# Kernel optimization log

Hardware: AMD Instinct MI355X
Metric: run time of the kernel (lower is better)

## Reference

```python
import jax, jax.numpy as jnp
import numpy as np
from math import pi as PI

K = 32
CUTOFF = 10.0
F = 128          # num_filters (also num_gaussians)
H = 256          # in_channels
N_CLASSES = 7
N_IND = 8
LOG2 = float(np.log(2.0))


def _ssp(x):
    # ShiftedSoftplus
    return jax.nn.softplus(x) - LOG2


def _gaussian_smearing(d):
    # d: [E, 1] -> [E, F]; torch_geometric GaussianSmearing(start=0, stop=cutoff)
    offset = jnp.linspace(0.0, CUTOFF, F, dtype=d.dtype)            # [F]
    coeff = -0.5 / (offset[1] - offset[0]) ** 2
    return jnp.exp(coeff * (d - offset[None, :]) ** 2)


def setup_inputs() -> dict:
    key = jax.random.key(0)
    ks = jax.random.split(key, 24)
    Nq, Nc, B = 8192, 16384, 8
    box = 20.0
    pos_query = jax.random.uniform(ks[0], (Nq, 3), dtype=jnp.float32) * box
    pos_ctx = jax.random.uniform(ks[1], (Nc, 3), dtype=jnp.float32) * box
    node_attr_ctx = jax.random.normal(ks[2], (Nc, H), dtype=jnp.float32)
    batch_query = jnp.sort(jax.random.randint(ks[3], (Nq,), 0, B)).astype(jnp.int32)
    batch_ctx = jnp.sort(jax.random.randint(ks[4], (Nc,), 0, B)).astype(jnp.int32)

    def lin_w(k, fin, fout):
        return (jax.random.normal(k, (fin, fout), dtype=jnp.float32) / np.sqrt(fin)).astype(jnp.float32)

    return {
        "pos_query": pos_query,
        "pos_ctx": pos_ctx,
        "node_attr_ctx": node_attr_ctx,
        "batch_query": batch_query,
        "batch_ctx": batch_ctx,
        "lin1_w": lin_w(ks[5], H, F),                 # bias=False
        "lin2_w": lin_w(ks[6], F, F),
        "lin2_b": jnp.zeros((F,), jnp.float32),
        "nn1_w": lin_w(ks[7], F, F),
        "nn1_b": jnp.zeros((F,), jnp.float32),
        "nn2_w": lin_w(ks[8], F, F),
        "nn2_b": jnp.zeros((F,), jnp.float32),
        "cls1_w": lin_w(ks[9], F, F),
        "cls1_b": jnp.zeros((F,), jnp.float32),
        "cls2_w": lin_w(ks[10], F, N_CLASSES),
        "cls2_b": jnp.zeros((N_CLASSES,), jnp.float32),
        "prop1_w": lin_w(ks[11], F, F),
        "prop1_b": jnp.zeros((F,), jnp.float32),
        "prop2_w": lin_w(ks[12], F, N_IND),
        "prop2_b": jnp.zeros((N_IND,), jnp.float32),
    }


def reference(pos_query, pos_ctx, node_attr_ctx, batch_query, batch_ctx,
              lin1_w, lin2_w, lin2_b, nn1_w, nn1_b, nn2_w, nn2_b,
              cls1_w, cls1_b, cls2_w, cls2_b, prop1_w, prop1_b, prop2_w, prop2_b):
    Nq = pos_query.shape[0]

    # --- batch-aware kNN: for each query, k nearest context points in same graph ---
    d2 = (jnp.sum(pos_query ** 2, -1)[:, None]
          + jnp.sum(pos_ctx ** 2, -1)[None, :]
          - 2.0 * (pos_query @ pos_ctx.T))                            # [Nq, Nc]
    same = batch_query[:, None] == batch_ctx[None, :]
    d2 = jnp.where(same, d2, jnp.inf)
    _, nbr = jax.lax.top_k(-d2, K)                                    # [Nq, K] ctx indices

    # --- gather neighbor data; each query owns exactly K contiguous edges ---
    diff = pos_query[:, None, :] - pos_ctx[nbr]                       # [Nq, K, 3]
    dist = jnp.sqrt(jnp.sum(diff ** 2, -1)).reshape(-1, 1)            # [E, 1]
    attr_j = node_attr_ctx[nbr].reshape(Nq * K, -1)                   # [E, H]

    # --- per-edge filter network on distance expansion ---
    W = _ssp(_gaussian_smearing(dist) @ nn1_w + nn1_b) @ nn2_w + nn2_b  # [E, F]

    h = (W * (attr_j @ lin1_w)) @ lin2_w + lin2_b                     # [E, F]

    # --- cosine cutoff envelope ---
    C = 0.5 * (jnp.cos(dist * (PI / CUTOFF)) + 1.0)
    C = C * (dist <= CUTOFF) * (dist >= 0.0)
    h = h * C                                                         # [E, F]

    # scatter_add by query index == sum over the K contiguous edges per query
    y = jnp.sum(h.reshape(Nq, K, F), axis=1)                          # [Nq, F]

    y_cls = _ssp(y @ cls1_w + cls1_b) @ cls2_w + cls2_b               # [Nq, 7]
    y_ind = _ssp(y @ prop1_w + prop1_b) @ prop2_w + prop2_b           # [Nq, 8]
    return (y_cls, y_ind)
```

## Files before the change

kernel.cpp:

```cpp
#include <hip/hip_runtime.h>
#include <math.h>

#define K 32
#define F 128
#define H 256
#define TAB 4096
#define QB 8
#define BMAX 16
#define RCUT2 100.0f
#define KBINS 64
#define BINCAP 2560
#define BCAP 128
#define FP 132
#define FRR 32
#define WRR 16

__device__ __forceinline__ float ssp(float x) {
    return fmaxf(x, 0.0f) + log1pf(expf(-fabsf(x))) - 0.69314718055994531f;
}

__device__ __forceinline__ float d2f4(float4 p, float qx, float qy, float qz) {
    float dx = qx - p.x;
    float dy = qy - p.y;
    float dz = qz - p.z;
    return fmaf(dz, dz, fmaf(dy, dy, dx * dx));
}

__global__ __launch_bounds__(256) void prep_kernel(const int* __restrict__ bc, int Nc,
                                                   int* __restrict__ ctx_start,
                                                   const float* __restrict__ posc,
                                                   float4* __restrict__ posc4) {
    int blk = blockIdx.x;
    int tid = threadIdx.x;
    if (blk == 0) {
        if (tid <= BMAX) {
            int b = tid;
            int lo = 0, hi = Nc;
            while (lo < hi) {
                int mid = (lo + hi) >> 1;
                if (bc[mid] < b) lo = mid + 1; else hi = mid;
            }
            ctx_start[b] = lo;
        }
    } else {
        int i = (blk - 1) * 256 + tid;
        if (i < Nc)
            posc4[i] = make_float4(posc[i * 3 + 0], posc[i * 3 + 1], posc[i * 3 + 2], 0.0f);
    }
}

__global__ __launch_bounds__(256) void feat_kernel(const float* __restrict__ attr,
                                                   const float* __restrict__ lin1_w,
                                                   float* __restrict__ ctx_feat, int Nc) {
    __shared__ float sa[FRR][H];
    int blk = blockIdx.x;
    int tid = threadIdx.x;
    int r0 = blk * FRR;
    int f = tid & 63;
    int g = tid >> 6;

    {
        float4* dst = (float4*)sa;
        const int total = FRR * H / 4;
        if (r0 + FRR <= Nc) {
            const float4* src = (const float4*)(attr + (size_t)r0 * H);
            for (int i = tid; i < total; i += 256) dst[i] = src[i];
        } else {
            for (int i = tid; i < total; i += 256) {
                int r = i / (H / 4);
                if (r0 + r < Nc) dst[i] = ((const float4*)(attr + (size_t)r0 * H))[i];
                else dst[i] = make_float4(0.0f, 0.0f, 0.0f, 0.0f);
            }
        }
    }
    __syncthreads();

    float acc0[8], acc1[8];
#pragma unroll
    for (int r = 0; r < 8; ++r) { acc0[r] = 0.0f; acc1[r] = 0.0f; }
    for (int k = 0; k < H; k += 4) {
        float wa0 = lin1_w[(k + 0) * F + f];
        float wa1 = lin1_w[(k + 1) * F + f];
        float wa2 = lin1_w[(k + 2) * F + f];
        float wa3 = lin1_w[(k + 3) * F + f];
        float wb0 = lin1_w[(k + 0) * F + f + 64];
        float wb1 = lin1_w[(k + 1) * F + f + 64];
        float wb2 = lin1_w[(k + 2) * F + f + 64];
        float wb3 = lin1_w[(k + 3) * F + f + 64];
#pragma unroll
        for (int r = 0; r < 8; ++r) {
            float4 a4 = *(const float4*)&sa[g * 8 + r][k];
            acc0[r] = fmaf(a4.x, wa0, acc0[r]);
            acc0[r] = fmaf(a4.y, wa1, acc0[r]);
            acc0[r] = fmaf(a4.z, wa2, acc0[r]);
            acc0[r] = fmaf(a4.w, wa3, acc0[r]);
            acc1[r] = fmaf(a4.x, wb0, acc1[r]);
            acc1[r] = fmaf(a4.y, wb1, acc1[r]);
            acc1[r] = fmaf(a4.z, wb2, acc1[r]);
            acc1[r] = fmaf(a4.w, wb3, acc1[r]);
        }
    }
#pragma unroll
    for (int r = 0; r < 8; ++r) {
        int row = r0 + g * 8 + r;
        if (row < Nc) {
            ctx_feat[(size_t)row * F + f] = acc0[r];
            ctx_feat[(size_t)row * F + f + 64] = acc1[r];
        }
    }
}

__global__ __launch_bounds__(256) void knn_kernel(const float* __restrict__ posq,
                                                  const float4* __restrict__ posc4,
                                                  const int* __restrict__ bq,
                                                  const int* __restrict__ ctx_start,
                                                  int* __restrict__ nbr, int Nq) {
    __shared__ unsigned char sbin[4][BINCAP];
    __shared__ int hist[4][KBINS];
    __shared__ unsigned bkey[4][BCAP];
    __shared__ int bidx[4][BCAP];
    __shared__ int s_nwin[4], s_nbnd[4];

    int tid = threadIdx.x;
    int lane = tid & 63;
    int w = tid >> 6;
    int q = blockIdx.x * 4 + w;
    bool active = q < Nq;
    int qc = active ? q : 0;

    hist[w][lane] = 0;
    if (lane == 0) { s_nwin[w] = 0; s_nbnd[w] = 0; }

    float qx = posq[qc * 3 + 0];
    float qy = posq[qc * 3 + 1];
    float qz = posq[qc * 3 + 2];
    int b = bq[qc];
    int c0 = ctx_start[b];
    int c1 = ctx_start[b + 1];
    int seg = active ? (c1 - c0) : 0;
    __syncthreads();

    const float SCALE = (float)KBINS / RCUT2;
    int farc = -1;

    for (int i = lane; i < seg; i += 64) {
        float d2 = d2f4(posc4[c0 + i], qx, qy, qz);
        int bin = 255;
        if (d2 < RCUT2) {
            bin = (int)(d2 * SCALE);
            atomicAdd(&hist[w][bin], 1);
        }
        if (i < BINCAP) sbin[w][i] = (unsigned char)bin;
    }
    __syncthreads();

    int h = hist[w][lane];
    int inc = h;
#pragma unroll
    for (int off = 1; off < 64; off <<= 1) {
        int v = __shfl_up(inc, off);
        if (lane >= off) inc += v;
    }
    unsigned long long bal = __ballot(inc >= K);
    int T, below;
    if (bal) {
        T = __ffsll(bal) - 1;
        below = __shfl(inc, T) - __shfl(h, T);
    } else {
        T = KBINS;
        below = __shfl(inc, 63);
    }

    for (int i = lane; i < seg; i += 64) {
        int c = c0 + i;
        int bin;
        if (i < BINCAP) bin = sbin[w][i];
        else {
            float d2 = d2f4(posc4[c], qx, qy, qz);
            bin = (d2 < RCUT2) ? (int)(d2 * SCALE) : 255;
        }
        if (bin < T) {
            int p = atomicAdd(&s_nwin[w], 1);
            nbr[(size_t)q * K + p] = c;
        } else if (bin == T) {
            int p = atomicAdd(&s_nbnd[w], 1);
            if (p < BCAP) {
                float d2 = d2f4(posc4[c], qx, qy, qz);
                bkey[w][p] = __float_as_uint(d2);
                bidx[w][p] = c;
            }
        } else if (bin == 255) {
            farc = c;
        }
    }
#pragma unroll
    for (int off = 1; off < 64; off <<= 1) farc = max(farc, __shfl_xor(farc, off));
    if (farc < 0) farc = c0;
    __syncthreads();

    if (!active) return;
    int nb = min(s_nbnd[w], BCAP);
    int m = K - s_nwin[w];
    for (int it = 0; it < m; ++it) {
        unsigned long long bestkey = 0xFFFFFFFFFFFFFFFFull;
        int bestp = -1;
        for (int p = lane; p < nb; p += 64) {
            unsigned kk = bkey[w][p];
            if (kk != 0xFFFFFFFFu) {
                unsigned long long pk = ((unsigned long long)kk << 32) | (unsigned)bidx[w][p];
                if (pk < bestkey) { bestkey = pk; bestp = p; }
            }
        }
#pragma unroll
        for (int off = 1; off < 64; off <<= 1) {
            unsigned long long ok = __shfl_xor(bestkey, off);
            int op = __shfl_xor(bestp, off);
            if (ok < bestkey) { bestkey = ok; bestp = op; }
        }
        if (lane == 0) {
            if (bestp >= 0 && bestkey != 0xFFFFFFFFFFFFFFFFull) {
                nbr[(size_t)q * K + below + it] = (int)(bestkey & 0xFFFFFFFFu);
                bkey[w][bestp] = 0xFFFFFFFFu;
            } else {
                nbr[(size_t)q * K + below + it] = farc;
            }
        }
        __asm__ volatile("" ::: "memory");
    }
}

__global__ __launch_bounds__(256) void wtab_kernel(const float* __restrict__ nn1_w,
                                                   const float* __restrict__ nn1_b,
                                                   const float* __restrict__ nn2_w,
                                                   const float* __restrict__ nn2_b,
                                                   float2* __restrict__ wt2) {
    __shared__ float sg[17][F];
    __shared__ float st[17][F];
    int t0 = blockIdx.x * WRR;
    int tid = threadIdx.x;
    int f = tid & (F - 1);
    int g = tid >> 7;

    const float delta = 10.0f / 127.0f;
    const float coeff = -0.5f / (delta * delta);
    float off = (float)f * delta;
    for (int r = g; r < 17; r += 2) {
        float dist = (float)(t0 + r) * (10.0f / (float)TAB);
        float d = dist - off;
        sg[r][f] = expf(coeff * d * d);
    }
    __syncthreads();

    float acc[9];
#pragma unroll
    for (int r = 0; r < 9; ++r) acc[r] = 0.0f;
    for (int j = 0; j < F; j += 4) {
        float w0 = nn1_w[(j + 0) * F + f];
        float w1 = nn1_w[(j + 1) * F + f];
        float w2 = nn1_w[(j + 2) * F + f];
        float w3 = nn1_w[(j + 3) * F + f];
#pragma unroll
        for (int r = 0; r < 9; ++r) {
            float4 a4 = *(const float4*)&sg[g * 8 + r][j];
            acc[r] = fmaf(a4.x, w0, acc[r]);
            acc[r] = fmaf(a4.y, w1, acc[r]);
            acc[r] = fmaf(a4.z, w2, acc[r]);
            acc[r] = fmaf(a4.w, w3, acc[r]);
        }
    }
    float b1 = nn1_b[f];
#pragma unroll
    for (int r = 0; r < 9; ++r) st[g * 8 + r][f] = ssp(acc[r] + b1);
    __syncthreads();

#pragma unroll
    for (int r = 0; r < 9; ++r) acc[r] = 0.0f;
    for (int j = 0; j < F; j += 4) {
        float w0 = nn2_w[(j + 0) * F + f];
        float w1 = nn2_w[(j + 1) * F + f];
        float w2 = nn2_w[(j + 2) * F + f];
        float w3 = nn2_w[(j + 3) * F + f];
#pragma unroll
        for (int r = 0; r < 9; ++r) {
            float4 a4 = *(const float4*)&st[g * 8 + r][j];
            acc[r] = fmaf(a4.x, w0, acc[r]);
            acc[r] = fmaf(a4.y, w1, acc[r]);
            acc[r] = fmaf(a4.z, w2, acc[r]);
            acc[r] = fmaf(a4.w, w3, acc[r]);
        }
    }
    float b2 = nn2_b[f];
#pragma unroll
    for (int i = 0; i < 8; ++i) {
        int t = t0 + g * 8 + i;
        wt2[(size_t)t * F + f] = make_float2(acc[i] + b2, acc[i + 1] + b2);
    }
}

__global__ __launch_bounds__(256) void agghead_kernel(const float* __restrict__ posq,
                                                      const float4* __restrict__ posc4,
                                                      const int* __restrict__ nbr,
                                                      const float* __restrict__ ctx_feat,
                                                      const float2* __restrict__ wt2,
                                                      const float* __restrict__ lin2_w,
                                                      const float* __restrict__ lin2_b,
                                                      const float* __restrict__ cls1_w,
                                                      const float* __restrict__ cls1_b,
                                                      const float* __restrict__ cls2_w,
                                                      const float* __restrict__ cls2_b,
                                                      const float* __restrict__ prop1_w,
                                                      const float* __restrict__ prop1_b,
                                                      const float* __restrict__ prop2_w,
                                                      const float* __restrict__ prop2_b,
                                                      float* __restrict__ out_cls,
                                                      float* __restrict__ out_ind, int Nq) {
    const int QH = QB / 2;
    int q0 = blockIdx.x * QB;
    int tid = threadIdx.x;

    __shared__ __align__(16) char sm[12672];
    float4* sedge      = (float4*)sm;
    float (*sa)[F]     = (float (*)[F])(sm + 4096);
    float* ssc         = (float*)(sm + 8192);
    float (*sc1)[FP]   = (float (*)[FP])(sm);
    float (*sp1)[FP]   = (float (*)[FP])(sm + 4224);
    float (*sy)[FP]    = (float (*)[FP])(sm + 8448);

    {
        int qq = tid >> 5;
        int q = q0 + qq;
        if (q >= Nq) q = Nq - 1;
        int j = nbr[(size_t)q * K + (tid & 31)];
        float4 p = posc4[j];
        float dx = posq[q * 3 + 0] - p.x;
        float dy = posq[q * 3 + 1] - p.y;
        float dz = posq[q * 3 + 2] - p.z;
        float dist = sqrtf(fmaf(dz, dz, fmaf(dy, dy, dx * dx)));
        float C = 0.0f, fr = 0.0f;
        int i0 = 0;
        if (dist <= 10.0f) {
            C = 0.5f * (cosf(dist * 0.31415926535897931f) + 1.0f);
            float u = dist * ((float)TAB / 10.0f);
            i0 = (int)u;
            if (i0 > TAB - 1) i0 = TAB - 1;
            fr = u - (float)i0;
        }
        sedge[tid] = make_float4(C, fr, __int_as_float(i0 * F), __int_as_float(j * F));
        float cs = C;
#pragma unroll
        for (int off = 1; off < 32; off <<= 1) cs += __shfl_xor(cs, off);
        if ((tid & 31) == 0) ssc[qq] = cs;
    }
    __syncthreads();

    int f = tid & (F - 1);
    int g = tid >> 7;

    {
        const float2* w2f = wt2 + f;
        const float* cff = ctx_feat + f;
        float acc[QH] = {0.0f, 0.0f, 0.0f, 0.0f};
#pragma unroll 2
        for (int k = 0; k < K; ++k) {
#pragma unroll
            for (int i = 0; i < QH; ++i) {
                float4 e4 = sedge[(g * QH + i) * K + k];
                float C = e4.x;
                float fr = e4.y;
                int i0f = __float_as_int(e4.z);
                int jf = __float_as_int(e4.w);
                float2 w = w2f[i0f];
                float a = cff[jf];
                float W = fmaf(fr, w.y - w.x, w.x);
                acc[i] = fmaf(C * W, a, acc[i]);
            }
        }
#pragma unroll
        for (int i = 0; i < QH; ++i) sa[g * QH + i][f] = acc[i];
    }
    __syncthreads();

    {
        float y[QH];
        float lb = lin2_b[f];
#pragma unroll
        for (int i = 0; i < QH; ++i) y[i] = ssc[g * QH + i] * lb;
        for (int j = 0; j < F; j += 4) {
            float w0 = lin2_w[(j + 0) * F + f];
            float w1 = lin2_w[(j + 1) * F + f];
            float w2 = lin2_w[(j + 2) * F + f];
            float w3 = lin2_w[(j + 3) * F + f];
#pragma unroll
            for (int i = 0; i < QH; ++i) {
                float4 a4 = *(const float4*)&sa[g * QH + i][j];
                y[i] = fmaf(a4.x, w0, y[i]);
                y[i] = fmaf(a4.y, w1, y[i]);
                y[i] = fmaf(a4.z, w2, y[i]);
                y[i] = fmaf(a4.w, w3, y[i]);
            }
        }
#pragma unroll
        for (int i = 0; i < QH; ++i) sy[g * QH + i][f] = y[i];
    }
    __syncthreads();

    {
        float c1[QH], p1[QH];
        float cb = cls1_b[f], pb = prop1_b[f];
#pragma unroll
        for (int i = 0; i < QH; ++i) { c1[i] = cb; p1[i] = pb; }
        for (int j = 0; j < F; j += 4) {
            float wc0 = cls1_w[(j + 0) * F + f];
            float wc1 = cls1_w[(j + 1) * F + f];
            float wc2 = cls1_w[(j + 2) * F + f];
            float wc3 = cls1_w[(j + 3) * F + f];
            float wp0 = prop1_w[(j + 0) * F + f];
            float wp1 = prop1_w[(j + 1) * F + f];
            float wp2 = prop1_w[(j + 2) * F + f];
            float wp3 = prop1_w[(j + 3) * F + f];
#pragma unroll
            for (int i = 0; i < QH; ++i) {
                float4 y4 = *(const float4*)&sy[g * QH + i][j];
                c1[i] = fmaf(y4.x, wc0, c1[i]);
                c1[i] = fmaf(y4.y, wc1, c1[i]);
                c1[i] = fmaf(y4.z, wc2, c1[i]);
                c1[i] = fmaf(y4.w, wc3, c1[i]);
                p1[i] = fmaf(y4.x, wp0, p1[i]);
                p1[i] = fmaf(y4.y, wp1, p1[i]);
                p1[i] = fmaf(y4.z, wp2, p1[i]);
                p1[i] = fmaf(y4.w, wp3, p1[i]);
            }
        }
#pragma unroll
        for (int i = 0; i < QH; ++i) {
            sc1[g * QH + i][f] = ssp(c1[i]);
            sp1[g * QH + i][f] = ssp(p1[i]);
        }
    }
    __syncthreads();

    {
        int qq = tid >> 5;
        int c = tid & 31;
        int q = q0 + qq;
        if (q < Nq && c < 15) {
            if (c < 7) {
                float acc = cls2_b[c];
                for (int j = 0; j < F; ++j) acc = fmaf(sc1[qq][j], cls2_w[j * 7 + c], acc);
                out_cls[(size_t)q * 7 + c] = acc;
            } else {
                int cc = c - 7;
                float acc = prop2_b[cc];
                for (int j = 0; j < F; ++j) acc = fmaf(sp1[qq][j], prop2_w[j * 8 + cc], acc);
                out_ind[(size_t)q * 8 + cc] = acc;
            }
        }
    }
}

extern "C" void kernel_launch(void* const* d_in, const int* in_sizes, int n_in,
                              void* d_out, int out_size, void* d_ws, size_t ws_size,
                              hipStream_t stream) {
    const float* posq   = (const float*)d_in[0];
    const float* posc   = (const float*)d_in[1];
    const float* attr   = (const float*)d_in[2];
    const int*   bq     = (const int*)d_in[3];
    const int*   bc     = (const int*)d_in[4];
    const float* lin1_w = (const float*)d_in[5];
    const float* lin2_w = (const float*)d_in[6];
    const float* lin2_b = (const float*)d_in[7];
    const float* nn1_w  = (const float*)d_in[8];
    const float* nn1_b  = (const float*)d_in[9];
    const float* nn2_w  = (const float*)d_in[10];
    const float* nn2_b  = (const float*)d_in[11];
    const float* cls1_w = (const float*)d_in[12];
    const float* cls1_b = (const float*)d_in[13];
    const float* cls2_w = (const float*)d_in[14];
    const float* cls2_b = (const float*)d_in[15];
    const float* prop1_w = (const float*)d_in[16];
    const float* prop1_b = (const float*)d_in[17];
    const float* prop2_w = (const float*)d_in[18];
    const float* prop2_b = (const float*)d_in[19];
    (void)n_in; (void)out_size; (void)ws_size;

    int Nq = in_sizes[0] / 3;
    int Nc = in_sizes[1] / 3;

    char* ws = (char*)d_ws;
    size_t off = 0;
    auto alloc = [&](size_t bytes) {
        off = (off + 255) & ~(size_t)255;
        void* p = ws + off;
        off += bytes;
        return p;
    };
    int*    ctx_start = (int*)alloc((BMAX + 1) * sizeof(int));
    int*    nbr       = (int*)alloc((size_t)Nq * K * sizeof(int));
    float*  ctx_feat  = (float*)alloc((size_t)Nc * F * sizeof(float));
    float2* wt2       = (float2*)alloc((size_t)TAB * F * sizeof(float2));
    float4* posc4     = (float4*)alloc((size_t)Nc * sizeof(float4));

    float* out_cls = (float*)d_out;
    float* out_ind = out_cls + (size_t)Nq * 7;

    int padB  = (Nc + 255) / 256;
    int featB = (Nc + FRR - 1) / FRR;
    int knnB  = (Nq + 3) / 4;
    int wtabB = TAB / WRR;

    prep_kernel<<<dim3(1 + padB), dim3(256), 0, stream>>>(bc, Nc, ctx_start, posc, posc4);
    knn_kernel<<<dim3(knnB), dim3(256), 0, stream>>>(posq, posc4, bq, ctx_start, nbr, Nq);
    feat_kernel<<<dim3(featB), dim3(256), 0, stream>>>(attr, lin1_w, ctx_feat, Nc);
    wtab_kernel<<<dim3(wtabB), dim3(256), 0, stream>>>(nn1_w, nn1_b, nn2_w, nn2_b, wt2);
    agghead_kernel<<<dim3((Nq + QB - 1) / QB), dim3(256), 0, stream>>>(
        posq, posc4, nbr, ctx_feat, wt2,
        lin2_w, lin2_b, cls1_w, cls1_b, cls2_w, cls2_b,
        prop1_w, prop1_b, prop2_w, prop2_b, out_cls, out_ind, Nq);
}
```

Baseline: 133.6 us.

## Reorder queries by Morton cell so agghead blocks share neighbor features

Computes a per-query key from batch id and a 16^3 Morton-coded spatial cell, then builds a query permutation with a histogram, single-block scan and atomic scatter. The aggregation kernel processes queries in this permuted order, so each block of 8 queries is spatially clustered and their neighbor ctx_feat rows overlap, improving cache reuse on gathers. This adds three small kernels and extra launches, plus one level of indirection for reading nbr and writing outputs.

```diff
diff --git a/kernel.cpp b/kernel.cpp
--- a/kernel.cpp
+++ b/kernel.cpp
@@ -14,6 +14,7 @@
 #define FP 132
 #define FRR 32
 #define WRR 16
+#define NCELL 32768
 
 __device__ __forceinline__ float ssp(float x) {
     return fmaxf(x, 0.0f) + log1pf(expf(-fabsf(x))) - 0.69314718055994531f;
@@ -26,10 +27,19 @@
     return fmaf(dz, dz, fmaf(dy, dy, dx * dx));
 }
 
+__device__ __forceinline__ unsigned ebits4(unsigned v) {
+    return (v & 1u) | ((v & 2u) << 2) | ((v & 4u) << 4) | ((v & 8u) << 6);
+}
+
 __global__ __launch_bounds__(256) void prep_kernel(const int* __restrict__ bc, int Nc,
                                                    int* __restrict__ ctx_start,
                                                    const float* __restrict__ posc,
-                                                   float4* __restrict__ posc4) {
+                                                   float4* __restrict__ posc4,
+                                                   const float* __restrict__ posq,
+                                                   const int* __restrict__ bq,
+                                                   int* __restrict__ qkey,
+                                                   int* __restrict__ ghist,
+                                                   int Nq, int padB, int qkB) {
     int blk = blockIdx.x;
     int tid = threadIdx.x;
     if (blk == 0) {
@@ -42,10 +52,61 @@
             }
             ctx_start[b] = lo;
         }
-    } else {
+    } else if (blk <= padB) {
         int i = (blk - 1) * 256 + tid;
         if (i < Nc)
             posc4[i] = make_float4(posc[i * 3 + 0], posc[i * 3 + 1], posc[i * 3 + 2], 0.0f);
+    } else if (blk <= padB + qkB) {
+        int q = (blk - 1 - padB) * 256 + tid;
+        if (q < Nq) {
+            float px = posq[q * 3 + 0], py = posq[q * 3 + 1], pz = posq[q * 3 + 2];
+            int xi = min(15, max(0, (int)(px * 0.8f)));
+            int yi = min(15, max(0, (int)(py * 0.8f)));
+            int zi = min(15, max(0, (int)(pz * 0.8f)));
+            unsigned m = ebits4((unsigned)xi) | (ebits4((unsigned)yi) << 1) | (ebits4((unsigned)zi) << 2);
+            qkey[q] = (bq[q] << 12) | (int)m;
+        }
+    } else {
+        int i = (blk - 1 - padB - qkB) * 256 + tid;
+        if (i < NCELL) ghist[i] = 0;
+    }
+}
+
+__global__ __launch_bounds__(256) void qhist_kernel(const int* __restrict__ qkey,
+                                                    int* __restrict__ ghist, int Nq) {
+    int q = blockIdx.x * 256 + threadIdx.x;
+    if (q < Nq) atomicAdd(&ghist[qkey[q]], 1);
+}
+
+__global__ __launch_bounds__(256) void qscan_kernel(int* __restrict__ ghist) {
+    __shared__ int part[256];
+    __shared__ int base[256];
+    int tid = threadIdx.x;
+    const int CH = NCELL / 256;
+    int s = 0;
+    for (int i = 0; i < CH; ++i) s += ghist[tid * CH + i];
+    part[tid] = s;
+    __syncthreads();
+    if (tid == 0) {
+        int run = 0;
+        for (int i = 0; i < 256; ++i) { base[i] = run; run += part[i]; }
+    }
+    __syncthreads();
+    int run = base[tid];
+    for (int i = 0; i < CH; ++i) {
+        int v = ghist[tid * CH + i];
+        ghist[tid * CH + i] = run;
+        run += v;
+    }
+}
+
+__global__ __launch_bounds__(256) void qscatter_kernel(const int* __restrict__ qkey,
+                                                       int* __restrict__ ghist,
+                                                       int* __restrict__ qperm, int Nq) {
+    int q = blockIdx.x * 256 + threadIdx.x;
+    if (q < Nq) {
+        int pos = atomicAdd(&ghist[qkey[q]], 1);
+        qperm[pos] = q;
     }
 }
 
@@ -302,6 +363,7 @@
                                                       const int* __restrict__ nbr,
                                                       const float* __restrict__ ctx_feat,
                                                       const float2* __restrict__ wt2,
+                                                      const int* __restrict__ qperm,
                                                       const float* __restrict__ lin2_w,
                                                       const float* __restrict__ lin2_b,
                                                       const float* __restrict__ cls1_w,
@@ -318,18 +380,21 @@
     int q0 = blockIdx.x * QB;
     int tid = threadIdx.x;
 
-    __shared__ __align__(16) char sm[12672];
+    __shared__ __align__(16) char sm[12704];
     float4* sedge      = (float4*)sm;
     float (*sa)[F]     = (float (*)[F])(sm + 4096);
     float* ssc         = (float*)(sm + 8192);
     float (*sc1)[FP]   = (float (*)[FP])(sm);
     float (*sp1)[FP]   = (float (*)[FP])(sm + 4224);
     float (*sy)[FP]    = (float (*)[FP])(sm + 8448);
+    int* sq            = (int*)(sm + 12672);
 
     {
         int qq = tid >> 5;
-        int q = q0 + qq;
-        if (q >= Nq) q = Nq - 1;
+        int qi = q0 + qq;
+        if (qi >= Nq) qi = Nq - 1;
+        int q = qperm[qi];
+        if ((tid & 31) == 0) sq[qq] = q;
         int j = nbr[(size_t)q * K + (tid & 31)];
         float4 p = posc4[j];
         float dx = posq[q * 3 + 0] - p.x;
@@ -442,8 +507,9 @@
     {
         int qq = tid >> 5;
         int c = tid & 31;
-        int q = q0 + qq;
-        if (q < Nq && c < 15) {
+        int qi = q0 + qq;
+        if (qi < Nq && c < 15) {
+            int q = sq[qq];
             if (c < 7) {
                 float acc = cls2_b[c];
                 for (int j = 0; j < F; ++j) acc = fmaf(sc1[qq][j], cls2_w[j * 7 + c], acc);
@@ -499,21 +565,30 @@
     float*  ctx_feat  = (float*)alloc((size_t)Nc * F * sizeof(float));
     float2* wt2       = (float2*)alloc((size_t)TAB * F * sizeof(float2));
     float4* posc4     = (float4*)alloc((size_t)Nc * sizeof(float4));
+    int*    qkey      = (int*)alloc((size_t)Nq * sizeof(int));
+    int*    ghist     = (int*)alloc((size_t)NCELL * sizeof(int));
+    int*    qperm     = (int*)alloc((size_t)Nq * sizeof(int));
 
     float* out_cls = (float*)d_out;
     float* out_ind = out_cls + (size_t)Nq * 7;
 
     int padB  = (Nc + 255) / 256;
+    int qkB   = (Nq + 255) / 256;
+    int zB    = (NCELL + 255) / 256;
     int featB = (Nc + FRR - 1) / FRR;
     int knnB  = (Nq + 3) / 4;
     int wtabB = TAB / WRR;
 
-    prep_kernel<<<dim3(1 + padB), dim3(256), 0, stream>>>(bc, Nc, ctx_start, posc, posc4);
+    prep_kernel<<<dim3(1 + padB + qkB + zB), dim3(256), 0, stream>>>(
+        bc, Nc, ctx_start, posc, posc4, posq, bq, qkey, ghist, Nq, padB, qkB);
+    qhist_kernel<<<dim3(qkB), dim3(256), 0, stream>>>(qkey, ghist, Nq);
+    qscan_kernel<<<dim3(1), dim3(256), 0, stream>>>(ghist);
+    qscatter_kernel<<<dim3(qkB), dim3(256), 0, stream>>>(qkey, ghist, qperm, Nq);
     knn_kernel<<<dim3(knnB), dim3(256), 0, stream>>>(posq, posc4, bq, ctx_start, nbr, Nq);
     feat_kernel<<<dim3(featB), dim3(256), 0, stream>>>(attr, lin1_w, ctx_feat, Nc);
     wtab_kernel<<<dim3(wtabB), dim3(256), 0, stream>>>(nn1_w, nn1_b, nn2_w, nn2_b, wt2);
     agghead_kernel<<<dim3((Nq + QB - 1) / QB), dim3(256), 0, stream>>>(
-        posq, posc4, nbr, ctx_feat, wt2,
+        posq, posc4, nbr, ctx_feat, wt2, qperm,
         lin2_w, lin2_b, cls1_w, cls1_b, cls2_w, cls2_b,
         prop1_w, prop1_b, prop2_w, prop2_b, out_cls, out_ind, Nq);
 }
```

New measurement: 155.1 us. 16.1% more time.
